# Performance work log

Measured on AMD Instinct MI355X. Metric: run time of the kernel, lower is better.

The kernel has to match this reference:

```python
import jax, jax.numpy as jnp
import numpy as np


def setup_inputs() -> dict:
    key = jax.random.key(0)
    k1, k2, k3 = jax.random.split(key, 3)
    B, N, D = 4, 4096, 256
    val = jax.random.normal(k1, (B, N, D), dtype=jnp.float32)
    state = jax.random.normal(k2, (B, N), dtype=jnp.float32)
    # val projection weight, scaled for unit-variance outputs
    Wv = jax.random.normal(k3, (D, D), dtype=jnp.float32) / np.sqrt(D)
    return {"val": val, "state": state, "Wv": Wv}


def reference(val, state, Wv):
    # pairwise_fn: dot-product scores over all node pairs -> [B, N, N]
    scores = jnp.einsum("bnd,bmd->bnm", val, val)
    # edge_compress_fn: softsign (non-softmax elementwise nonlinearity)
    edges = scores / (1.0 + jnp.abs(scores))
    # state_proj_fn = identity, val_proj_fn = linear
    projected_state = state                                  # [B, N]
    projected_val = jnp.einsum("bmd,de->bme", val, Wv)       # [B, N, D]
    # dual aggregation reusing the same edge matrix
    delta_state = jnp.einsum("bnm,bm->bn", edges, projected_state)
    delta_val = jnp.einsum("bnm,bmd->bnd", edges, projected_val)
    return (delta_state, delta_val)
```

## Files before the change

### kernel.cpp

```cpp
#include <hip/hip_runtime.h>

typedef unsigned short u16;
typedef unsigned char u8;
typedef unsigned int u32;
typedef __bf16 bf16x8 __attribute__((ext_vector_type(8)));
typedef float  f32x16 __attribute__((ext_vector_type(16)));
typedef int    i32x4  __attribute__((ext_vector_type(4)));
typedef int    i32x16 __attribute__((ext_vector_type(16)));

#define NB 4
#define NN 4096
#define ND 256

#define QPV (127.0f / 4.5f)
#define DPV (4.5f / 16129.0f)
#define QST (127.0f / 4.6f)
#define DST (4.6f / 16129.0f)
#define MAGIC 12582912.0f

__device__ __forceinline__ u16 f2bf(float x) { return __builtin_bit_cast(u16, (__bf16)x); }
__device__ __forceinline__ u32 fbits(float x) { return __builtin_bit_cast(u32, x); }

__device__ __forceinline__ u32 packlow4(float a, float b, float c, float d) {
    u32 p = __builtin_amdgcn_perm(fbits(b), fbits(a), 0x00000400u);
    u32 q = __builtin_amdgcn_perm(fbits(d), fbits(c), 0x00000400u);
    return __builtin_amdgcn_perm(q, p, 0x05040100u);
}


__global__ __launch_bounds__(256) void k_misc(const float* __restrict__ Wv,
                                              const float* __restrict__ state,
                                              u16* __restrict__ wv, u8* __restrict__ vp8) {
    int tid = threadIdx.x;
    int bid = blockIdx.x;
    if (bid < 8) {
        __shared__ u16 t2[256 * 33];
        int es = bid, e0 = es * 32;
        #pragma unroll
        for (int k = 0; k < 8; k++) {
            int idx = tid + k * 256;
            int row = idx >> 3, c4 = idx & 7;
            float4 v = *(const float4*)(Wv + row * 256 + e0 + c4 * 4);
            u16* p = t2 + row * 33 + c4 * 4;
            p[0] = f2bf(v.x); p[1] = f2bf(v.y); p[2] = f2bf(v.z); p[3] = f2bf(v.w);
        }
        __syncthreads();
        u16* dst = wv + (size_t)es * 16 * 512;
        #pragma unroll
        for (int k = 0; k < 4; k++) {
            int flat = tid + k * 256;
            int s = flat >> 6, l = flat & 63;
            int l31 = l & 31, h = l >> 5;
            union { u16 o[8]; uint4 q; } u;
            #pragma unroll
            for (int j = 0; j < 8; j++) u.o[j] = t2[(s * 16 + h * 8 + j) * 33 + l31];
            *(uint4*)(dst + (size_t)flat * 8) = u.q;
        }
    } else {
        int b = bid - 8;
        __shared__ u8 qs[4096];
        #pragma unroll
        for (int k = 0; k < 16; k++) {
            int i = tid + k * 256;
            float x = fminf(fmaxf(state[b * 4096 + i] * QST, -127.0f), 127.0f);
            qs[i] = (u8)(fbits(x + MAGIC) & 255);
        }
        __syncthreads();
        #pragma unroll
        for (int k = 0; k < 32; k++) {
            int chunk = tid + k * 256;
            int strip = chunk >> 6, lane = chunk & 63, h = (lane >> 5) & 1;
            i32x4 v = *(const i32x4*)(qs + strip * 32 + h * 16);
            *(i32x4*)(vp8 + ((size_t)((b * 128 + strip) * 9 + 8)) * 1024 + (chunk & 63) * 16) = v;
        }
    }
}

#define TFS 260
__global__ __launch_bounds__(256) void k_pv2(const float* __restrict__ val,
                                             const u16* __restrict__ wv,
                                             u8* __restrict__ kq8, u8* __restrict__ vp8,
                                             float* __restrict__ srow) {
    __shared__ float tf[64 * TFS];
    __shared__ float rmax[64];
    __shared__ u8 tp[4][32 * 48];

    int tid = threadIdx.x;
    int w = tid >> 6, lane = tid & 63;
    int l31 = lane & 31, h = lane >> 5;
    int bs = blockIdx.x;

    const float* src = val + (size_t)bs * 64 * 256;
    #pragma unroll
    for (int k = 0; k < 16; k++) {
        int idx = tid + k * 256;
        int row = idx >> 6, c4 = idx & 63;
        float4 v = *(const float4*)(src + row * 256 + c4 * 4);
        *(float4*)(tf + row * TFS + c4 * 4) = v;
    }
    __syncthreads();

    {
        int row = tid >> 2, seg = tid & 3;
        float m = 0.0f;
        #pragma unroll
        for (int i = 0; i < 16; i++) {
            float4 v = *(const float4*)(tf + row * TFS + seg * 4 + i * 16);
            m = fmaxf(fmaxf(fabsf(v.x), fabsf(v.y)), fmaxf(fmaxf(fabsf(v.z), fabsf(v.w)), m));
        }
        m = fmaxf(m, __shfl_xor(m, 1));
        m = fmaxf(m, __shfl_xor(m, 2));
        if (seg == 0) {
            m = fmaxf(m, 1e-20f);
            rmax[row] = m;
            srow[bs * 64 + row] = m * (1.0f / 127.0f);
        }
    }
    __syncthreads();

    #pragma unroll
    for (int k = 0; k < 4; k++) {
        int flat = tid + k * 256;
        int strip = flat >> 9, rest = flat & 511;
        int s = rest >> 6, l = rest & 63;
        int fl31 = l & 31, fh = l >> 5;
        int row = strip * 32 + fl31;
        float r127 = 127.0f / rmax[row];
        const float* p = tf + row * TFS + s * 32 + fh * 16;
        u32 d[4];
        #pragma unroll
        for (int g = 0; g < 4; g++)
            d[g] = packlow4(fmaf(p[4 * g + 0], r127, MAGIC), fmaf(p[4 * g + 1], r127, MAGIC),
                            fmaf(p[4 * g + 2], r127, MAGIC), fmaf(p[4 * g + 3], r127, MAGIC));
        *(uint4*)(kq8 + ((size_t)(bs * 2 + strip)) * 8192 + (size_t)(s * 64 + l) * 16) =
            make_uint4(d[0], d[1], d[2], d[3]);
    }

    f32x16 acc[2][2] = {};
    for (int s = 0; s < 16; s++) {
        bf16x8 bq[2];
        #pragma unroll
        for (int qt = 0; qt < 2; qt++) {
            const float* p = tf + (qt * 32 + l31) * TFS + s * 16 + h * 8;
            union { __bf16 e[8]; bf16x8 v; } u;
            #pragma unroll
            for (int j = 0; j < 8; j++) u.e[j] = (__bf16)p[j];
            bq[qt] = u.v;
        }
        #pragma unroll
        for (int ei = 0; ei < 2; ei++) {
            int es = w * 2 + ei;
            bf16x8 af = *(const bf16x8*)(wv + (size_t)(es * 16 + s) * 512 + lane * 8);
            acc[ei][0] = __builtin_amdgcn_mfma_f32_32x32x16_bf16(af, bq[0], acc[ei][0], 0, 0, 0);
            acc[ei][1] = __builtin_amdgcn_mfma_f32_32x32x16_bf16(af, bq[1], acc[ei][1], 0, 0, 0);
        }
    }
    u8* myp = tp[w];
    #pragma unroll
    for (int ei = 0; ei < 2; ei++) {
        int es = w * 2 + ei;
        #pragma unroll
        for (int qt = 0; qt < 2; qt++) {
            #pragma unroll
            for (int r = 0; r < 16; r++) {
                int erow = (r & 3) + 8 * (r >> 2) + 4 * h;
                float x = fminf(fmaxf(acc[ei][qt][r] * QPV, -127.0f), 127.0f);
                myp[erow * 48 + l31] = (u8)(fbits(x + MAGIC) & 255);
            }
            i32x4 v = *(const i32x4*)(myp + l31 * 48 + h * 16);
            *(i32x4*)(vp8 + ((size_t)((bs * 2 + qt) * 9 + es)) * 1024 + lane * 16) = v;
        }
    }
}

__global__ __launch_bounds__(512, 2) void k_main(const u8* __restrict__ kq8,
                                                 const u8* __restrict__ vp8,
                                                 const float* __restrict__ srow,
                                                 float* __restrict__ ds_out,
                                                 float* __restrict__ dval_out) {
    __shared__ int red[2 * 8192];
    __shared__ int dsqi[2][4][32];

    int tid = threadIdx.x;
    int w = tid >> 6, lane = tid & 63;
    int l31 = lane & 31, h = lane >> 5;
    int strip = w & 1, mq = w >> 1;

    int id = blockIdx.x;
    int xcd = id & 7;
    int bb = xcd >> 1;
    int t6 = ((xcd & 1) << 5) | (id >> 3);
    int q0 = t6 * 64;
    size_t bbase = (size_t)bb * 128;

    i32x4 qf[8];
    {
        const u8* qsrc = kq8 + (bbase + t6 * 2 + strip) * 8192 + lane * 16;
        #pragma unroll
        for (int s = 0; s < 8; s++) qf[s] = *(const i32x4*)(qsrc + (size_t)s * 1024);
    }
    float srq = srow[bb * 4096 + q0 + strip * 32 + l31];

    i32x16 oacc[8] = {};
    i32x16 dsa = {};

    for (int mt = 0; mt < 32; mt++) {
        const u8* kb = kq8 + (bbase + mt * 4 + mq) * 8192 + lane * 16;
        const u8* vbG = vp8 + (bbase + mt * 4 + mq) * 9216 + lane * 16;
        i32x4 kf[8];
        #pragma unroll
        for (int s = 0; s < 8; s++) kf[s] = *(const i32x4*)(kb + (size_t)s * 1024);
        const float* srm = srow + bb * 4096 + mt * 128 + mq * 32;
        float4 sg[4];
        #pragma unroll
        for (int g = 0; g < 4; g++) sg[g] = *(const float4*)(srm + g * 8 + h * 4);

        i32x16 sacc = {};
        #pragma unroll
        for (int s = 0; s < 8; s++)
            sacc = __builtin_amdgcn_mfma_i32_32x32x32_i8(kf[s], qf[s], sacc, 0, 0, 0);

        float cf[16];
        #pragma unroll
        for (int r = 0; r < 16; r++) {
            float sm = ((const float*)&sg[r >> 2])[r & 3] * srq;
            float xs = (float)sacc[r] * sm;
            float p = xs * __builtin_amdgcn_rcpf(1.0f + fabsf(xs));
            cf[r] = fmaf(p, 127.0f, MAGIC);
        }
        u32 w0 = packlow4(cf[0], cf[1], cf[2], cf[3]);
        u32 w1 = packlow4(cf[4], cf[5], cf[6], cf[7]);
        u32 w2 = packlow4(cf[8], cf[9], cf[10], cf[11]);
        u32 w3 = packlow4(cf[12], cf[13], cf[14], cf[15]);
        u32 x0 = (u32)__shfl_xor((int)w0, 32);
        u32 x1 = (u32)__shfl_xor((int)w1, 32);
        u32 x2 = (u32)__shfl_xor((int)w2, 32);
        u32 x3 = (u32)__shfl_xor((int)w3, 32);
        union { u32 wd[4]; i32x4 v; } pu;
        if (h == 0) { pu.wd[0] = w0; pu.wd[1] = x0; pu.wd[2] = w1; pu.wd[3] = x1; }
        else        { pu.wd[0] = x2; pu.wd[1] = w2; pu.wd[2] = x3; pu.wd[3] = w3; }
        i32x4 pf = pu.v;

        #pragma unroll
        for (int et = 0; et < 8; et++) {
            i32x4 vf = *(const i32x4*)(vbG + (size_t)et * 1024);
            oacc[et] = __builtin_amdgcn_mfma_i32_32x32x32_i8(pf, vf, oacc[et], 0, 0, 0);
        }
        {
            i32x4 sf = *(const i32x4*)(vbG + (size_t)8 * 1024);
            dsa = __builtin_amdgcn_mfma_i32_32x32x32_i8(pf, sf, dsa, 0, 0, 0);
        }
    }

    __syncthreads();
    if (l31 == 0) {
        #pragma unroll
        for (int r = 0; r < 16; r++) dsqi[strip][mq][(r & 3) + 8 * (r >> 2) + 4 * h] = dsa[r];
    }
    int* rd = red + strip * 8192;
    if (mq == 3) {
        #pragma unroll
        for (int et = 0; et < 8; et++)
            #pragma unroll
            for (int r = 0; r < 16; r++) {
                int row = (r & 3) + 8 * (r >> 2) + 4 * h;
                rd[row * 256 + et * 32 + l31] = oacc[et][r];
            }
    }
    __syncthreads();
    if (mq == 2) {
        #pragma unroll
        for (int et = 0; et < 8; et++)
            #pragma unroll
            for (int r = 0; r < 16; r++) {
                int row = (r & 3) + 8 * (r >> 2) + 4 * h;
                rd[row * 256 + et * 32 + l31] += oacc[et][r];
            }
    }
    __syncthreads();
    if (mq == 1) {
        #pragma unroll
        for (int et = 0; et < 8; et++)
            #pragma unroll
            for (int r = 0; r < 16; r++) {
                int row = (r & 3) + 8 * (r >> 2) + 4 * h;
                rd[row * 256 + et * 32 + l31] += oacc[et][r];
            }
    }
    __syncthreads();
    if (mq == 0) {
        #pragma unroll
        for (int et = 0; et < 8; et++)
            #pragma unroll
            for (int r = 0; r < 16; r++) {
                int row = (r & 3) + 8 * (r >> 2) + 4 * h;
                int sum = oacc[et][r] + rd[row * 256 + et * 32 + l31];
                dval_out[((size_t)(bb * 4096 + q0 + strip * 32 + row)) * 256 + et * 32 + l31] =
                    (float)sum * DPV;
            }
        if (lane < 32) {
            int d = dsqi[strip][0][lane] + dsqi[strip][1][lane] +
                    dsqi[strip][2][lane] + dsqi[strip][3][lane];
            ds_out[bb * 4096 + q0 + strip * 32 + lane] = (float)d * DST;
        }
    }
}

extern "C" void kernel_launch(void* const* d_in, const int* in_sizes, int n_in,
                              void* d_out, int out_size, void* d_ws, size_t ws_size,
                              hipStream_t stream) {
    const float* val   = (const float*)d_in[0];
    const float* state = (const float*)d_in[1];
    const float* Wv    = (const float*)d_in[2];

    float* ds_out   = (float*)d_out;
    float* dval_out = ds_out + NB * NN;

    u8*  kq8 = (u8*)d_ws;
    u8*  vp8 = kq8 + (size_t)NB * NN * ND;
    u16* wv  = (u16*)(vp8 + (size_t)NB * 128 * 9216);
    float* srow = (float*)(wv + 8 * 16 * 512);

    k_misc<<<12, 256, 0, stream>>>(Wv, state, wv, vp8);
    k_pv2<<<256, 256, 0, stream>>>(val, wv, kq8, vp8, srow);
    k_main<<<256, 512, 0, stream>>>(kq8, vp8, srow, ds_out, dval_out);
}
```

Measured before the change: 155.2 us.

## Split main kernel by output half and stage V tiles via async LDS loads

The main kernel now runs 1024 blocks of 4 waves instead of 256 blocks of 8. Each block handles one 32-row query strip and one half of the output columns. Per-tile V fragments are prefetched into double-buffered shared memory with global_load_lds, replacing direct global loads in the inner loop. This aims to improve occupancy and overlap memory with MFMA work. The cost is that each block recomputes the full score tile and softsign for its half, so the QK^T work is duplicated twice.

```diff
diff --git a/kernel.cpp b/kernel.cpp
--- a/kernel.cpp
+++ b/kernel.cpp
@@ -25,6 +25,12 @@
     u32 p = __builtin_amdgcn_perm(fbits(b), fbits(a), 0x00000400u);
     u32 q = __builtin_amdgcn_perm(fbits(d), fbits(c), 0x00000400u);
     return __builtin_amdgcn_perm(q, p, 0x05040100u);
+}
+
+typedef __attribute__((address_space(1))) const u32 gas_u32;
+typedef __attribute__((address_space(3))) u32 las_u32;
+__device__ __forceinline__ void async_ld16(void* lds, const void* g) {
+    __builtin_amdgcn_global_load_lds((gas_u32*)g, (las_u32*)lds, 16, 0, 0);
 }
 
 
@@ -173,135 +179,175 @@
     }
 }
 
-__global__ __launch_bounds__(512, 2) void k_main(const u8* __restrict__ kq8,
+__global__ __launch_bounds__(256, 3) void k_main(const u8* __restrict__ kq8,
                                                  const u8* __restrict__ vp8,
                                                  const float* __restrict__ srow,
                                                  float* __restrict__ ds_out,
                                                  float* __restrict__ dval_out) {
-    __shared__ int red[2 * 8192];
-    __shared__ int dsqi[2][4][32];
+    __shared__ u8 stage[2][4][5120];
+    __shared__ int dsqi[4][32];
 
     int tid = threadIdx.x;
-    int w = tid >> 6, lane = tid & 63;
+    int mq = tid >> 6, lane = tid & 63;
     int l31 = lane & 31, h = lane >> 5;
-    int strip = w & 1, mq = w >> 1;
 
     int id = blockIdx.x;
     int xcd = id & 7;
     int bb = xcd >> 1;
-    int t6 = ((xcd & 1) << 5) | (id >> 3);
-    int q0 = t6 * 64;
+    int eh = (id >> 3) & 1;
+    int t7 = ((xcd & 1) << 6) | (id >> 4);
+    int q0 = t7 * 32;
     size_t bbase = (size_t)bb * 128;
 
     i32x4 qf[8];
     {
-        const u8* qsrc = kq8 + (bbase + t6 * 2 + strip) * 8192 + lane * 16;
+        const u8* qsrc = kq8 + (bbase + t7) * 8192 + lane * 16;
         #pragma unroll
         for (int s = 0; s < 8; s++) qf[s] = *(const i32x4*)(qsrc + (size_t)s * 1024);
     }
-    float srq = srow[bb * 4096 + q0 + strip * 32 + l31];
-
-    i32x16 oacc[8] = {};
+    float srq = srow[bb * 4096 + q0 + l31];
+
+    i32x16 oacc[4] = {};
     i32x16 dsa = {};
+
+    int nslots = 4 + (eh == 0 ? 1 : 0);
+    {
+        const u8* sv = vp8 + (bbase + mq) * 9216;
+        #pragma unroll
+        for (int k = 0; k < 5; k++) {
+            if (k >= nslots) break;
+            int ss = (k < 4) ? (eh * 4 + k) : 8;
+            async_ld16(&stage[0][mq][(size_t)k * 1024 + lane * 16],
+                       sv + (size_t)ss * 1024 + lane * 16);
+        }
+    }
 
     for (int mt = 0; mt < 32; mt++) {
         const u8* kb = kq8 + (bbase + mt * 4 + mq) * 8192 + lane * 16;
-        const u8* vbG = vp8 + (bbase + mt * 4 + mq) * 9216 + lane * 16;
-        i32x4 kf[8];
-        #pragma unroll
-        for (int s = 0; s < 8; s++) kf[s] = *(const i32x4*)(kb + (size_t)s * 1024);
+        i32x4 kf0[4], kf1[4];
+        #pragma unroll
+        for (int s = 0; s < 4; s++) kf0[s] = *(const i32x4*)(kb + (size_t)s * 1024);
+        #pragma unroll
+        for (int s = 0; s < 4; s++) kf1[s] = *(const i32x4*)(kb + (size_t)(4 + s) * 1024);
         const float* srm = srow + bb * 4096 + mt * 128 + mq * 32;
         float4 sg[4];
         #pragma unroll
         for (int g = 0; g < 4; g++) sg[g] = *(const float4*)(srm + g * 8 + h * 4);
+        if (mt + 1 < 32) {
+            const u8* sv = vp8 + (bbase + (mt + 1) * 4 + mq) * 9216;
+            #pragma unroll
+            for (int k = 0; k < 5; k++) {
+                if (k >= nslots) break;
+                int ss = (k < 4) ? (eh * 4 + k) : 8;
+                async_ld16(&stage[(mt + 1) & 1][mq][(size_t)k * 1024 + lane * 16],
+                           sv + (size_t)ss * 1024 + lane * 16);
+            }
+        }
 
         i32x16 sacc = {};
         #pragma unroll
-        for (int s = 0; s < 8; s++)
-            sacc = __builtin_amdgcn_mfma_i32_32x32x32_i8(kf[s], qf[s], sacc, 0, 0, 0);
-
-        float cf[16];
-        #pragma unroll
-        for (int r = 0; r < 16; r++) {
-            float sm = ((const float*)&sg[r >> 2])[r & 3] * srq;
-            float xs = (float)sacc[r] * sm;
-            float p = xs * __builtin_amdgcn_rcpf(1.0f + fabsf(xs));
-            cf[r] = fmaf(p, 127.0f, MAGIC);
-        }
-        u32 w0 = packlow4(cf[0], cf[1], cf[2], cf[3]);
-        u32 w1 = packlow4(cf[4], cf[5], cf[6], cf[7]);
-        u32 w2 = packlow4(cf[8], cf[9], cf[10], cf[11]);
-        u32 w3 = packlow4(cf[12], cf[13], cf[14], cf[15]);
-        u32 x0 = (u32)__shfl_xor((int)w0, 32);
-        u32 x1 = (u32)__shfl_xor((int)w1, 32);
-        u32 x2 = (u32)__shfl_xor((int)w2, 32);
-        u32 x3 = (u32)__shfl_xor((int)w3, 32);
-        union { u32 wd[4]; i32x4 v; } pu;
-        if (h == 0) { pu.wd[0] = w0; pu.wd[1] = x0; pu.wd[2] = w1; pu.wd[3] = x1; }
-        else        { pu.wd[0] = x2; pu.wd[1] = w2; pu.wd[2] = x3; pu.wd[3] = w3; }
+        for (int s = 0; s < 4; s++)
+            sacc = __builtin_amdgcn_mfma_i32_32x32x32_i8(kf0[s], qf[s], sacc, 0, 0, 0);
+        #pragma unroll
+        for (int s = 0; s < 4; s++)
+            sacc = __builtin_amdgcn_mfma_i32_32x32x32_i8(kf1[s], qf[4 + s], sacc, 0, 0, 0);
+
+        u32 wd[4];
+        #pragma unroll
+        for (int g = 0; g < 4; g++) {
+            float c0, c1, c2, c3;
+            {
+                float sm = ((const float*)&sg[g])[0] * srq;
+                float xs = (float)sacc[4 * g + 0] * sm;
+                c0 = fmaf(xs * __builtin_amdgcn_rcpf(1.0f + fabsf(xs)), 127.0f, MAGIC);
+            }
+            {
+                float sm = ((const float*)&sg[g])[1] * srq;
+                float xs = (float)sacc[4 * g + 1] * sm;
+                c1 = fmaf(xs * __builtin_amdgcn_rcpf(1.0f + fabsf(xs)), 127.0f, MAGIC);
+            }
+            {
+                float sm = ((const float*)&sg[g])[2] * srq;
+                float xs = (float)sacc[4 * g + 2] * sm;
+                c2 = fmaf(xs * __builtin_amdgcn_rcpf(1.0f + fabsf(xs)), 127.0f, MAGIC);
+            }
+            {
+                float sm = ((const float*)&sg[g])[3] * srq;
+                float xs = (float)sacc[4 * g + 3] * sm;
+                c3 = fmaf(xs * __builtin_amdgcn_rcpf(1.0f + fabsf(xs)), 127.0f, MAGIC);
+            }
+            wd[g] = packlow4(c0, c1, c2, c3);
+        }
+        u32 x0 = (u32)__shfl_xor((int)wd[0], 32);
+        u32 x1 = (u32)__shfl_xor((int)wd[1], 32);
+        u32 x2 = (u32)__shfl_xor((int)wd[2], 32);
+        u32 x3 = (u32)__shfl_xor((int)wd[3], 32);
+        union { u32 w[4]; i32x4 v; } pu;
+        if (h == 0) { pu.w[0] = wd[0]; pu.w[1] = x0; pu.w[2] = wd[1]; pu.w[3] = x1; }
+        else        { pu.w[0] = x2; pu.w[1] = wd[2]; pu.w[2] = x3; pu.w[3] = wd[3]; }
         i32x4 pf = pu.v;
 
-        #pragma unroll
-        for (int et = 0; et < 8; et++) {
-            i32x4 vf = *(const i32x4*)(vbG + (size_t)et * 1024);
+        const u8* vb = stage[mt & 1][mq];
+        #pragma unroll
+        for (int et = 0; et < 4; et++) {
+            i32x4 vf = *(const i32x4*)(vb + et * 1024 + lane * 16);
             oacc[et] = __builtin_amdgcn_mfma_i32_32x32x32_i8(pf, vf, oacc[et], 0, 0, 0);
         }
-        {
-            i32x4 sf = *(const i32x4*)(vbG + (size_t)8 * 1024);
+        if (eh == 0) {
+            i32x4 sf = *(const i32x4*)(vb + 4 * 1024 + lane * 16);
             dsa = __builtin_amdgcn_mfma_i32_32x32x32_i8(pf, sf, dsa, 0, 0, 0);
         }
     }
 
     __syncthreads();
-    if (l31 == 0) {
-        #pragma unroll
-        for (int r = 0; r < 16; r++) dsqi[strip][mq][(r & 3) + 8 * (r >> 2) + 4 * h] = dsa[r];
-    }
-    int* rd = red + strip * 8192;
+    if (eh == 0 && l31 == 0) {
+        #pragma unroll
+        for (int r = 0; r < 16; r++) dsqi[mq][(r & 3) + 8 * (r >> 2) + 4 * h] = dsa[r];
+    }
+    int* red = (int*)stage;
     if (mq == 3) {
         #pragma unroll
-        for (int et = 0; et < 8; et++)
+        for (int et = 0; et < 4; et++)
             #pragma unroll
             for (int r = 0; r < 16; r++) {
                 int row = (r & 3) + 8 * (r >> 2) + 4 * h;
-                rd[row * 256 + et * 32 + l31] = oacc[et][r];
+                red[row * 128 + et * 32 + l31] = oacc[et][r];
             }
     }
     __syncthreads();
     if (mq == 2) {
         #pragma unroll
-        for (int et = 0; et < 8; et++)
+        for (int et = 0; et < 4; et++)
             #pragma unroll
             for (int r = 0; r < 16; r++) {
                 int row = (r & 3) + 8 * (r >> 2) + 4 * h;
-                rd[row * 256 + et * 32 + l31] += oacc[et][r];
+                red[row * 128 + et * 32 + l31] += oacc[et][r];
             }
     }
     __syncthreads();
     if (mq == 1) {
         #pragma unroll
-        for (int et = 0; et < 8; et++)
+        for (int et = 0; et < 4; et++)
             #pragma unroll
             for (int r = 0; r < 16; r++) {
                 int row = (r & 3) + 8 * (r >> 2) + 4 * h;
-                rd[row * 256 + et * 32 + l31] += oacc[et][r];
+                red[row * 128 + et * 32 + l31] += oacc[et][r];
             }
     }
     __syncthreads();
     if (mq == 0) {
         #pragma unroll
-        for (int et = 0; et < 8; et++)
+        for (int et = 0; et < 4; et++)
             #pragma unroll
             for (int r = 0; r < 16; r++) {
                 int row = (r & 3) + 8 * (r >> 2) + 4 * h;
-                int sum = oacc[et][r] + rd[row * 256 + et * 32 + l31];
-                dval_out[((size_t)(bb * 4096 + q0 + strip * 32 + row)) * 256 + et * 32 + l31] =
+                int sum = oacc[et][r] + red[row * 128 + et * 32 + l31];
+                dval_out[((size_t)(bb * 4096 + q0 + row)) * 256 + eh * 128 + et * 32 + l31] =
                     (float)sum * DPV;
             }
-        if (lane < 32) {
-            int d = dsqi[strip][0][lane] + dsqi[strip][1][lane] +
-                    dsqi[strip][2][lane] + dsqi[strip][3][lane];
-            ds_out[bb * 4096 + q0 + strip * 32 + lane] = (float)d * DST;
+        if (eh == 0 && lane < 32) {
+            int d = dsqi[0][lane] + dsqi[1][lane] + dsqi[2][lane] + dsqi[3][lane];
+            ds_out[bb * 4096 + q0 + lane] = (float)d * DST;
         }
     }
 }
@@ -323,5 +369,5 @@
 
     k_misc<<<12, 256, 0, stream>>>(Wv, state, wv, vp8);
     k_pv2<<<256, 256, 0, stream>>>(val, wv, kq8, vp8, srow);
-    k_main<<<256, 512, 0, stream>>>(kq8, vp8, srow, ds_out, dval_out);
-}
+    k_main<<<1024, 256, 0, stream>>>(kq8, vp8, srow, ds_out, dval_out);
+}
```

Result: slower. 292.6 us (+88.5%).
